# Optimization experiments

Measured on AMD Instinct MI355X. Metric: run time of the kernel, lower is better.

## Reference

```python
import jax, jax.numpy as jnp
import numpy as np

B, N, H, KRATE = 128, 400, 128, 0.2
EPS = 1e-9


def setup_inputs() -> dict:
    key = jax.random.key(0)
    ks = jax.random.split(key, 16)
    # correlation-like input: symmetric, values in (-1,1), unit diagonal
    x = jax.random.normal(ks[0], (B, N, N), dtype=jnp.float32)
    x = jnp.tanh(0.3 * x)
    x = 0.5 * (x + x.transpose(0, 2, 1))
    eye = jnp.eye(N, dtype=jnp.float32)
    x = x * (1.0 - eye) + eye

    def lin(k, fan_in, shape):
        return jax.random.normal(k, shape, dtype=jnp.float32) / np.sqrt(fan_in).astype(np.float32)

    return {
        "x": x,
        "slength": jnp.full((B,), 100, dtype=jnp.int32),
        # AE denoiser (num_of_node=N, hidden=H)
        "enc1_w": lin(ks[1], N, (N, H)), "enc1_b": jnp.zeros((H,), jnp.float32),
        "enc2_w": lin(ks[2], N, (N, H)), "enc2_b": jnp.zeros((H,), jnp.float32),
        "dec2_w": lin(ks[3], H, (H, N)), "dec2_b": jnp.zeros((N,), jnp.float32),
        "dec1_w": lin(ks[4], H, (H, N)), "dec1_b": jnp.zeros((N,), jnp.float32),
        # GCN predictor
        "gcn1_w": lin(ks[5], N, (N, H)), "gcn1_b": jnp.zeros((H,), jnp.float32),
        "gcn2_w": lin(ks[6], H, (H, H)), "gcn2_b": jnp.zeros((H,), jnp.float32),
        # classification head Linear(128 -> 2)
        "fc_w": lin(ks[7], H, (H, 2)), "fc_b": jnp.zeros((2,), jnp.float32),
    }


def reference(x, slength, enc1_w, enc1_b, enc2_w, enc2_b, dec2_w, dec2_b,
              dec1_w, dec1_b, gcn1_w, gcn1_b, gcn2_w, gcn2_b, fc_w, fc_b):
    eye = jnp.eye(N, dtype=x.dtype)

    # fisher transform + normalize by [0,0] entry
    xf = 0.5 * jnp.log((1.0 + x + EPS) / (1.0 - x + EPS))
    xf = xf / xf[:, 0, 0][:, None, None]

    # --- DA / AE denoiser: deltax = AE(xf), symmetrized ---
    out1 = jax.nn.relu(jnp.einsum('bij,jh->bih', xf, enc1_w) + enc1_b).transpose(0, 2, 1)  # [B,H,N]
    out2 = jax.nn.relu(jnp.einsum('bhn,nk->bhk', out1, enc2_w) + enc2_b)                   # [B,H,H]
    out2 = jax.nn.relu(jnp.einsum('bhk,kn->bhn', out2, dec2_w) + dec2_b + out1)            # [B,H,N]
    out2 = out2.transpose(0, 2, 1)                                                         # [B,N,H]
    delta = jnp.einsum('bnh,hm->bnm', out2, dec1_w) + dec1_b                               # [B,N,N]
    delta = 0.5 * (delta + delta.transpose(0, 2, 1))
    x2 = xf + delta * (1.0 - eye)

    # --- predictor on detached x2 ---
    xp = jax.lax.stop_gradient(x2)

    # topk sparsification at rate 0.2 over flattened NxN per sample
    k = int(N * N * KRATE)
    flat = xp.reshape(B, N * N)
    _, idx = jax.lax.top_k(flat, k)
    mask = jnp.zeros((B, N * N), xp.dtype).at[jnp.arange(B)[:, None], idx].set(1.0)
    A = xp * mask.reshape(B, N, N)

    # GCN norm (PyG gcn_norm with add_remaining_self_loops, fill=1)
    diag = jnp.diagonal(A, axis1=1, axis2=2)
    A = A + eye[None] * jnp.where(diag == 0.0, 1.0, 0.0)[:, :, None]
    deg = A.sum(axis=1)                      # scatter of edge weight on col index
    dinv = deg ** -0.5
    dinv = jnp.where(jnp.isinf(dinv), 0.0, dinv)
    An = dinv[:, :, None] * A * dinv[:, None, :]  # An[b,i,j] = dinv[i]*A[i,j]*dinv[j]

    # GCNConv1 -> ReLU -> GCNConv2 (aggregate onto col/target index)
    h = jax.nn.relu(jnp.einsum('bij,bif->bjf', An, xp @ gcn1_w) + gcn1_b)  # [B,N,H]
    h = jnp.einsum('bij,bif->bjf', An, h @ gcn2_w) + gcn2_b                # [B,N,H]

    pooled = h.mean(axis=1)                  # mean over nodes -> [B,H]
    out = jax.nn.relu(pooled) @ fc_w + fc_b  # [B,2]
    return out
```

## Files before the change

kernel.cpp:

```cpp
#include <hip/hip_runtime.h>
#include <hip/hip_bf16.h>
#include <math.h>

#define BATCH 128
#define NNODE 400
#define HID   128
#define NN    (NNODE*NNODE)
#define KSEL  32000
#define EQCAP 1024
#define EPSF  1e-9f
#define TSPLIT 8
#define SEG   (NN / TSPLIT)
#define NT    7
#define KC400 14
#define FRAGS (KC400*4096)
#define PLA   57344

__device__ __forceinline__ unsigned tokey(float f) {
  unsigned u = __float_as_uint(f);
  return (u & 0x80000000u) ? ~u : (u | 0x80000000u);
}

__device__ __forceinline__ short f2bf(float f) {
  unsigned u = __float_as_uint(f);
  u += 0x7fffu + ((u >> 16) & 1u);
  return (short)(u >> 16);
}
__device__ __forceinline__ float bf2f(short s) {
  return __uint_as_float(((unsigned)(unsigned short)s) << 16);
}

__device__ __forceinline__ float xfhw(float xv, float cmul) {
  float la = __builtin_amdgcn_logf(1.0f + xv + EPSF);
  float lb = __builtin_amdgcn_logf(1.0f - xv + EPSF);
  return (la - lb) * cmul;
}

typedef __attribute__((ext_vector_type(8))) short s8v;
typedef __attribute__((ext_vector_type(4))) short s4v;
typedef __attribute__((ext_vector_type(4))) float f4v;

#define BK 16
#define LP 68

template<bool AT, bool BIAS, bool RES, bool RELU, bool TS>
__global__ void __launch_bounds__(256) gemm64(
    const float* __restrict__ A, long sA, int lda,
    const float* __restrict__ B, long sB, int ldb,
    const float* __restrict__ bias,
    const float* __restrict__ Res, long sRes,
    float* __restrict__ C, long sC, int ldc,
    int M, int Nc, int K)
{
  __shared__ float As[BK][LP];
  __shared__ float Bs[BK][LP];
  const int bz = blockIdx.z;
  A += (size_t)bz * sA;
  B += (size_t)bz * sB;
  C += (size_t)bz * sC;
  const float* Rp = RES ? (Res + (size_t)bz * sRes) : nullptr;

  const int n0 = blockIdx.x * 64;
  const int m0 = blockIdx.y * 64;
  const int tid = threadIdx.x;
  const int tx = tid & 15, ty = tid >> 4;
  const bool edgeM = (m0 + 64 > M);
  const bool edgeN = (n0 + 64 > Nc);

  float acc[4][4];
#pragma unroll
  for (int i = 0; i < 4; ++i)
#pragma unroll
    for (int j = 0; j < 4; ++j) acc[i][j] = 0.f;

  for (int k0 = 0; k0 < K; k0 += BK) {
    if (!AT) {
      const int m = tid & 63, g = tid >> 6;
      if (!edgeM) {
        const float4 v = *(const float4*)(A + (size_t)(m0 + m) * lda + k0 + 4 * g);
        As[4 * g + 0][m] = v.x; As[4 * g + 1][m] = v.y;
        As[4 * g + 2][m] = v.z; As[4 * g + 3][m] = v.w;
      } else {
        const int gm = m0 + m;
        const bool ok = gm < M;
#pragma unroll
        for (int j = 0; j < 4; ++j)
          As[4 * g + j][m] = ok ? A[(size_t)gm * lda + k0 + 4 * g + j] : 0.f;
      }
    } else {
      const int k = tid >> 4, mg = tid & 15;
      if (!edgeM) {
        const float4 v = *(const float4*)(A + (size_t)(k0 + k) * lda + m0 + 4 * mg);
        *(float4*)&As[k][4 * mg] = v;
      } else {
#pragma unroll
        for (int j = 0; j < 4; ++j) {
          const int gm = m0 + 4 * mg + j;
          As[k][4 * mg + j] = (gm < M) ? A[(size_t)(k0 + k) * lda + gm] : 0.f;
        }
      }
    }
    {
      const int k = tid >> 4, ng = tid & 15;
      if (!edgeN) {
        const float4 v = *(const float4*)(B + (size_t)(k0 + k) * ldb + n0 + 4 * ng);
        *(float4*)&Bs[k][4 * ng] = v;
      } else {
#pragma unroll
        for (int j = 0; j < 4; ++j) {
          const int gn = n0 + 4 * ng + j;
          Bs[k][4 * ng + j] = (gn < Nc) ? B[(size_t)(k0 + k) * ldb + gn] : 0.f;
        }
      }
    }
    __syncthreads();
#pragma unroll
    for (int kk = 0; kk < BK; ++kk) {
      const float4 a = *(const float4*)&As[kk][ty << 2];
      const float4 b = *(const float4*)&Bs[kk][tx << 2];
      const float av[4] = {a.x, a.y, a.z, a.w};
      const float bv[4] = {b.x, b.y, b.z, b.w};
#pragma unroll
      for (int i = 0; i < 4; ++i)
#pragma unroll
        for (int j = 0; j < 4; ++j) acc[i][j] += av[i] * bv[j];
    }
    __syncthreads();
  }

#pragma unroll
  for (int i = 0; i < 4; ++i) {
    const int m = m0 + (ty << 2) + i;
    if (m >= M) continue;
#pragma unroll
    for (int j = 0; j < 4; ++j) {
      const int n = n0 + (tx << 2) + j;
      if (n >= Nc) continue;
      float v = acc[i][j];
      if (BIAS) v += bias[n];
      const size_t loc = TS ? ((size_t)n * ldc + m) : ((size_t)m * ldc + n);
      if (RES) v += Rp[loc];
      if (RELU) v = fmaxf(v, 0.f);
      C[loc] = v;
    }
  }
}

__global__ void bsplitN(const float* __restrict__ W, int K, int Kpad,
                        int N, int Npad, short* __restrict__ out) {
  int t = blockIdx.x * 256 + threadIdx.x;
  if (t >= Kpad * Npad) return;
  int k = t / Npad, n = t - k * Npad;
  float v = (k < K && n < N) ? W[(size_t)k * N + n] : 0.f;
  short hi = f2bf(v);
  short lo = f2bf(v - bf2f(hi));
  int ntiles = Npad >> 4;
  size_t idx = (((size_t)(k >> 5) * ntiles + (n >> 4)) * 64
                + (((k >> 3) & 3) * 16 + (n & 15))) * 8 + (k & 7);
  size_t PL = (size_t)(Kpad >> 5) * ntiles * 512;
  out[idx] = hi;
  out[PL + idx] = lo;
}

template<bool AT, bool FRAG, bool BIAS, bool RELU, bool SCL, bool TS, bool XF>
__global__ void __launch_bounds__(256) mfgemm(
    const float* __restrict__ A, long sA, int lda,
    const short* __restrict__ Bf, long sB, int kc,
    const float* __restrict__ bias,
    const float* __restrict__ scl,
    float* __restrict__ Cf, long sCf, int ldc,
    short* __restrict__ Cfrag, long sCfrag, int okc,
    const float* __restrict__ denomp, float* __restrict__ xfout,
    int M, int K)
{
  __shared__ float As[64][68];
  const int bz = blockIdx.y;
  A += (size_t)bz * sA;
  Bf += (size_t)bz * sB;
  if (SCL) scl += (size_t)bz * NNODE;
  if (!FRAG) Cf += (size_t)bz * sCf;
  else       Cfrag += (size_t)bz * sCfrag;
  if (XF) xfout += (size_t)bz * sA;
  const float cmul = XF ? (0.34657359027997264f / denomp[bz]) : 0.f;

  const int tid = threadIdx.x;
  const int lane = tid & 63, wave = tid >> 6;
  const int wqm = wave >> 1, wqn = wave & 1;
  const int quad = lane >> 4, l15 = lane & 15;
  const int m0 = blockIdx.x * 64;

  f4v acc[2][4];
#pragma unroll
  for (int i = 0; i < 2; ++i)
#pragma unroll
    for (int j = 0; j < 4; ++j) acc[i][j] = (f4v){0.f, 0.f, 0.f, 0.f};

  const int nstage = (K + 63) >> 6;
  for (int st = 0; st < nstage; ++st) {
    const int k0 = st << 6;
    if (st) __syncthreads();
    if (!AT) {
      const int mrow = tid >> 4;
      const int k4 = (tid & 15) << 2;
#pragma unroll
      for (int u = 0; u < 4; ++u) {
        const int m = mrow + (u << 4);
        const int gm = m0 + m, gk = k0 + k4;
        float4 v = {0.f, 0.f, 0.f, 0.f};
        if (gm < M) {
          if (gk + 4 <= K) {
            float4 xv = *(const float4*)(A + (size_t)gm * lda + gk);
            if (XF) {
              v.x = xfhw(xv.x, cmul);
              v.y = xfhw(xv.y, cmul);
              v.z = xfhw(xv.z, cmul);
              v.w = xfhw(xv.w, cmul);
              *(float4*)(xfout + (size_t)gm * lda + gk) = v;
            } else v = xv;
          } else {
            float* pv = (float*)&v;
#pragma unroll
            for (int j = 0; j < 4; ++j)
              if (gk + j < K) {
                float xv = A[(size_t)gm * lda + gk + j];
                if (XF) {
                  pv[j] = xfhw(xv, cmul);
                  xfout[(size_t)gm * lda + gk + j] = pv[j];
                } else pv[j] = xv;
              }
          }
        }
        *(float4*)&As[m][k4] = v;
      }
    } else {
      const int kk = tid >> 4;
      const int m4 = (tid & 15) << 2;
#pragma unroll
      for (int u = 0; u < 4; ++u) {
        const int gk = k0 + kk + (u << 4);
        float4 v = {0.f, 0.f, 0.f, 0.f};
        if (gk < K) {
          if (m0 + m4 + 4 <= M) v = *(const float4*)(A + (size_t)gk * lda + m0 + m4);
          else {
            float* pv = (float*)&v;
#pragma unroll
            for (int j = 0; j < 4; ++j)
              if (m0 + m4 + j < M) pv[j] = A[(size_t)gk * lda + m0 + m4 + j];
          }
        }
        As[m4 + 0][kk + (u << 4)] = v.x;
        As[m4 + 1][kk + (u << 4)] = v.y;
        As[m4 + 2][kk + (u << 4)] = v.z;
        As[m4 + 3][kk + (u << 4)] = v.w;
      }
    }
    __syncthreads();

#pragma unroll
    for (int c2 = 0; c2 < 2; ++c2) {
      const int c = (st << 1) + c2;
      s8v bhi[4], blo[4];
#pragma unroll
      for (int nt = 0; nt < 4; ++nt) {
        const int ntg = (wqn << 2) + nt;
        const size_t off = (((size_t)c * 8 + ntg) * 64 + lane) * 8;
        bhi[nt] = *(const s8v*)(Bf + off);
        blo[nt] = *(const s8v*)(Bf + (size_t)kc * 4096 + off);
      }
#pragma unroll
      for (int mt = 0; mt < 2; ++mt) {
        const int row = (wqm << 5) + (mt << 4) + l15;
        const int kof = (c2 << 5) + (quad << 3);
        const f4v a0 = *(const f4v*)&As[row][kof];
        const f4v a1 = *(const f4v*)&As[row][kof + 4];
        s8v ah, al;
#pragma unroll
        for (int j = 0; j < 4; ++j) {
          short h0 = f2bf(a0[j]); ah[j] = h0; al[j] = f2bf(a0[j] - bf2f(h0));
          short h1 = f2bf(a1[j]); ah[j + 4] = h1; al[j + 4] = f2bf(a1[j] - bf2f(h1));
        }
#pragma unroll
        for (int nt = 0; nt < 4; ++nt) {
          acc[mt][nt] = __builtin_amdgcn_mfma_f32_16x16x32_bf16(ah, bhi[nt], acc[mt][nt], 0, 0, 0);
          acc[mt][nt] = __builtin_amdgcn_mfma_f32_16x16x32_bf16(ah, blo[nt], acc[mt][nt], 0, 0, 0);
          acc[mt][nt] = __builtin_amdgcn_mfma_f32_16x16x32_bf16(al, bhi[nt], acc[mt][nt], 0, 0, 0);
        }
      }
    }
  }

  if (TS) {
    for (int nh = 0; nh < 2; ++nh) {
      __syncthreads();
      if (wqn == nh) {
#pragma unroll
        for (int mt = 0; mt < 2; ++mt)
#pragma unroll
          for (int nt = 0; nt < 4; ++nt) {
            const int tn = (nt << 4) + l15;
            const int n  = (wqn << 6) + tn;
            const int mc = (wqm << 5) + (mt << 4) + (quad << 2);
            const f4v a = acc[mt][nt];
#pragma unroll
            for (int reg = 0; reg < 4; ++reg) {
              float v = a[reg];
              if (SCL) v *= scl[m0 + mc + reg];
              if (BIAS) v += bias[n];
              if (RELU) v = fmaxf(v, 0.f);
              As[tn][mc + reg] = v;
            }
          }
      }
      __syncthreads();
      const int row = tid >> 2, cq = tid & 3;
#pragma unroll
      for (int u = 0; u < 4; ++u) {
        const int col = (cq + (u << 2)) << 2;
        if (m0 + col + 4 <= M) {
          const float4 v = *(const float4*)&As[row][col];
          *(float4*)(Cf + (size_t)((nh << 6) + row) * ldc + m0 + col) = v;
        }
      }
    }
    return;
  }

#pragma unroll
  for (int mt = 0; mt < 2; ++mt) {
    const int mb = m0 + (wqm << 5) + (mt << 4) + (quad << 2);
#pragma unroll
    for (int nt = 0; nt < 4; ++nt) {
      const int n = (wqn << 6) + (nt << 4) + l15;
      const f4v a = acc[mt][nt];
      if (!FRAG) {
#pragma unroll
        for (int reg = 0; reg < 4; ++reg) {
          const int m = mb + reg;
          if (m < M) {
            float v = a[reg];
            if (SCL) v *= scl[m];
            if (BIAS) v += bias[n];
            if (RELU) v = fmaxf(v, 0.f);
            Cf[(size_t)m * ldc + n] = v;
          }
        }
      } else {
        s4v h4, l4;
#pragma unroll
        for (int reg = 0; reg < 4; ++reg) {
          const int m = mb + reg;
          float v = (m < M) ? (SCL ? a[reg] * scl[m] : a[reg]) : 0.f;
          short hh = f2bf(v);
          h4[reg] = hh; l4[reg] = f2bf(v - bf2f(hh));
        }
        const int chunkT = mb >> 5, quadT = (mb >> 3) & 3, jT0 = mb & 7;
        const size_t off = (((size_t)chunkT * 8 + (wqn << 2) + nt) * 64
                            + quadT * 16 + l15) * 8 + jT0;
        *(s4v*)(Cfrag + off) = h4;
        *(s4v*)(Cfrag + (size_t)okc * 4096 + off) = l4;
      }
    }
  }
}

__global__ void __launch_bounds__(256) g4mf(
    const float* __restrict__ o1,
    const short* __restrict__ wfrag,
    const float* __restrict__ bias,
    float* __restrict__ xf,
    unsigned* __restrict__ ghist)
{
  __shared__ float D2[64][68];
  __shared__ unsigned hist[2304];
  const int b = blockIdx.y;
  int p = blockIdx.x, bi = 0;
  while (p >= NT - bi) { p -= NT - bi; ++bi; }
  const int bj = bi + p;
  const int I0 = bi * 64, J0 = bj * 64;
  const bool diag = (bi == bj);

  o1 += (size_t)b * HID * NNODE;
  xf += (size_t)b * NN;
  unsigned* gh = ghist + b * 256;

  const int tid = threadIdx.x;
  const int lane = tid & 63, wave = tid >> 6;
  const int wq = wave & 1;
  const bool d1 = wave < 2;
  const int Bt = (d1 ? bj : bi) * 4;
  const int quad = lane >> 4, l15 = lane & 15;
  const int M0 = d1 ? I0 : J0;

  for (int i = tid; i < 2304; i += 256) hist[i] = 0u;

  f4v acc[2][4];
#pragma unroll
  for (int i = 0; i < 2; ++i)
#pragma unroll
    for (int j = 0; j < 4; ++j) acc[i][j] = (f4v){0.f, 0.f, 0.f, 0.f};

  const int gm0 = M0 + (wq << 5) + l15;

  for (int c = 0; c < 4; ++c) {
    const int k0 = c << 5;
    s8v bhi[4], blo[4];
#pragma unroll
    for (int nt = 0; nt < 4; ++nt) {
      const int ntg = Bt + nt;
      const size_t off = (((size_t)c * 28 + ntg) * 64 + lane) * 8;
      bhi[nt] = *(const s8v*)(wfrag + off);
      blo[nt] = *(const s8v*)(wfrag + PLA + off);
    }
#pragma unroll
    for (int mt = 0; mt < 2; ++mt) {
      const int gm = gm0 + (mt << 4);
      float av[8];
      if (gm < NNODE) {
        const float* cp = o1 + (size_t)(k0 + (quad << 3)) * NNODE + gm;
#pragma unroll
        for (int j = 0; j < 8; ++j) av[j] = cp[(size_t)j * NNODE];
      } else {
#pragma unroll
        for (int j = 0; j < 8; ++j) av[j] = 0.f;
      }
      s8v ah, al;
#pragma unroll
      for (int j = 0; j < 8; ++j) {
        short h = f2bf(av[j]); ah[j] = h; al[j] = f2bf(av[j] - bf2f(h));
      }
#pragma unroll
      for (int nt = 0; nt < 4; ++nt) {
        acc[mt][nt] = __builtin_amdgcn_mfma_f32_16x16x32_bf16(ah, bhi[nt], acc[mt][nt], 0, 0, 0);
        acc[mt][nt] = __builtin_amdgcn_mfma_f32_16x16x32_bf16(ah, blo[nt], acc[mt][nt], 0, 0, 0);
        acc[mt][nt] = __builtin_amdgcn_mfma_f32_16x16x32_bf16(al, bhi[nt], acc[mt][nt], 0, 0, 0);
      }
    }
  }

  if (!d1) {
#pragma unroll
    for (int mt = 0; mt < 2; ++mt) {
      const int mb = (wq << 5) + (mt << 4) + (quad << 2);
#pragma unroll
      for (int nt = 0; nt < 4; ++nt) {
        const int nn = (nt << 4) + l15;
        const f4v a = acc[mt][nt];
#pragma unroll
        for (int reg = 0; reg < 4; ++reg) D2[mb + reg][nn] = a[reg];
      }
    }
  }
  __syncthreads();

  if (d1) {
    const int rep = tid & 7;
#pragma unroll
    for (int mt = 0; mt < 2; ++mt) {
      const int a0 = (wq << 5) + (mt << 4) + (quad << 2);
#pragma unroll
      for (int nt = 0; nt < 4; ++nt) {
        const int nn = (nt << 4) + l15;
        const int gj = J0 + nn;
        const f4v d1v = acc[mt][nt];
        const f4v d2t = *(const f4v*)&D2[nn][a0];
        f4v vv;
#pragma unroll
        for (int reg = 0; reg < 4; ++reg) {
          const int gi = I0 + a0 + reg;
          float v = 0.f;
          if (gi < NNODE && gj < NNODE) {
            v = xf[(size_t)gi * NNODE + gj];
            if (gi != gj)
              v += 0.5f * (d1v[reg] + d2t[reg] + bias[gj] + bias[gi]);
            atomicAdd(&hist[(tokey(v) >> 24) * 9 + rep], diag ? 1u : 2u);
          }
          vv[reg] = v;
        }
#pragma unroll
        for (int reg = 0; reg < 4; ++reg) {
          const int gi = I0 + a0 + reg;
          if (gi < NNODE && gj < NNODE) xf[(size_t)gi * NNODE + gj] = vv[reg];
        }
        if (!diag && gj < NNODE && (I0 + a0 + 4 <= NNODE)) {
          *(float4*)(xf + (size_t)gj * NNODE + I0 + a0) = *(float4*)&vv;
        }
      }
    }
  }
  __syncthreads();
  if (tid < 256) {
    const int hb = tid * 9;
    const unsigned s = hist[hb + 0] + hist[hb + 1] + hist[hb + 2] + hist[hb + 3]
                     + hist[hb + 4] + hist[hb + 5] + hist[hb + 6] + hist[hb + 7];
    if (s) atomicAdd(&gh[tid], s);
  }
}

__global__ void denom_k(const float* __restrict__ x, float* __restrict__ denom) {
  int b = threadIdx.x;
  if (b < BATCH) {
    float v = x[(size_t)b * NN];
    denom[b] = 0.5f * logf((1.0f + v + EPSF) / (1.0f - v + EPSF));
  }
}

__global__ void tz_init(unsigned* __restrict__ ghist, unsigned* __restrict__ sprefix,
                        int* __restrict__ sk, int* __restrict__ eqcnt,
                        float* __restrict__ deg) {
  int t = blockIdx.x * 256 + threadIdx.x;
  if (t < BATCH * 256) ghist[t] = 0u;
  if (t < BATCH) { sprefix[t] = 0u; sk[t] = KSEL; eqcnt[t] = 0; }
  if (t < BATCH * NNODE) deg[t] = 0.f;
}

template<int PASS>
__global__ void __launch_bounds__(256) thist(const float* __restrict__ x2,
                                             const unsigned* __restrict__ sprefix,
                                             unsigned* __restrict__ ghist) {
  constexpr int shift = 24 - 8 * PASS;
  __shared__ unsigned h[8][256];
  const int b  = blockIdx.y;
  const int sb = blockIdx.x;
  const int tid = threadIdx.x;
  for (int i = tid; i < 8 * 256; i += 256) ((unsigned*)h)[i] = 0u;
  __syncthreads();

  const unsigned prefix = sprefix[b];
  const unsigned pmask  = 0xFFFFFFFFu << (shift + 8);
  const int rep = tid & 7;
  const float4* p4 = (const float4*)(x2 + (size_t)b * NN);
  const int i0 = sb * (SEG / 4), i1 = i0 + (SEG / 4);
  for (int i = i0 + tid; i < i1; i += 256) {
    float4 v = p4[i];
    unsigned k0 = tokey(v.x), k1 = tokey(v.y), k2 = tokey(v.z), k3 = tokey(v.w);
    if ((k0 & pmask) == prefix) atomicAdd(&h[rep][(k0 >> shift) & 255u], 1u);
    if ((k1 & pmask) == prefix) atomicAdd(&h[rep][(k1 >> shift) & 255u], 1u);
    if ((k2 & pmask) == prefix) atomicAdd(&h[rep][(k2 >> shift) & 255u], 1u);
    if ((k3 & pmask) == prefix) atomicAdd(&h[rep][(k3 >> shift) & 255u], 1u);
  }
  __syncthreads();
  if (tid < 256) {
    unsigned s = h[0][tid] + h[1][tid] + h[2][tid] + h[3][tid]
               + h[4][tid] + h[5][tid] + h[6][tid] + h[7][tid];
    if (s) atomicAdd(&ghist[b * 256 + tid], s);
  }
}

template<int PASS>
__global__ void __launch_bounds__(256) tpick(unsigned* __restrict__ ghist,
                                             unsigned* __restrict__ sprefix,
                                             int* __restrict__ sk,
                                             unsigned* __restrict__ tau,
                                             int* __restrict__ rrem) {
  constexpr int shift = 24 - 8 * PASS;
  const int b = blockIdx.x;
  __shared__ unsigned h[256];
  h[threadIdx.x] = ghist[b * 256 + threadIdx.x];
  __syncthreads();
  if (threadIdx.x == 0) {
    int k = sk[b];
    unsigned byte = 0u;
    for (int bin = 255; bin >= 0; --bin) {
      int c = (int)h[bin];
      if (c >= k) { byte = (unsigned)bin; break; }
      k -= c;
    }
    unsigned np = sprefix[b] | (byte << shift);
    sprefix[b] = np; sk[b] = k;
    if (PASS == 3) { tau[b] = np; rrem[b] = k; }
  }
  ghist[b * 256 + threadIdx.x] = 0u;
}

__global__ void __launch_bounds__(256) build_kc(
    const float* __restrict__ x2, const unsigned* __restrict__ tau,
    float* __restrict__ A, float* __restrict__ deg,
    int* __restrict__ eqcnt, int* __restrict__ eqidx) {
  __shared__ float cs[NNODE];
  const int b = blockIdx.y, rg = blockIdx.x;
  const int tid = threadIdx.x;
  for (int i = tid; i < NNODE; i += 256) cs[i] = 0.f;
  __syncthreads();
  const unsigned tk = tau[b];
  const size_t base = (size_t)b * NN + (size_t)rg * 6400;
  for (int u = 0; u < 25; ++u) {
    const int t = u * 256 + tid;
    const float v = x2[base + t];
    const unsigned key = tokey(v);
    const float a = (key > tk) ? v : 0.f;
    A[base + t] = a;
    if (key == tk) {
      int p = atomicAdd(&eqcnt[b], 1);
      if (p < EQCAP) eqidx[b * EQCAP + p] = rg * 6400 + t;
    }
    if (a != 0.f) atomicAdd(&cs[t % NNODE], a);
  }
  __syncthreads();
  for (int j = tid; j < NNODE; j += 256)
    if (cs[j] != 0.f) atomicAdd(&deg[b * NNODE + j], cs[j]);
}

__global__ void eqfix_k(float* __restrict__ A, const float* __restrict__ x2,
                        float* __restrict__ deg,
                        const int* __restrict__ eqcnt, const int* __restrict__ eqidx,
                        const int* __restrict__ rrem) {
  int b = blockIdx.x;
  int cnt = eqcnt[b]; if (cnt > EQCAP) cnt = EQCAP;
  int r = rrem[b];
  for (int t = threadIdx.x; t < cnt; t += 256) {
    int idx = eqidx[b * EQCAP + t];
    int rank = 0;
    for (int u = 0; u < cnt; ++u) rank += (eqidx[b * EQCAP + u] < idx) ? 1 : 0;
    if (rank < r) {
      float v = x2[(size_t)b * NN + idx];
      A[(size_t)b * NN + idx] = v;
      atomicAdd(&deg[b * NNODE + idx % NNODE], v);
    }
  }
}

__global__ void dinv_k(float* __restrict__ A, const float* __restrict__ deg,
                       float* __restrict__ dinv) {
  int t = blockIdx.x * blockDim.x + threadIdx.x;
  if (t >= BATCH * NNODE) return;
  int b = t / NNODE, j = t - b * NNODE;
  float d = deg[t];
  size_t o = (size_t)b * NN + (size_t)j * NNODE + j;
  if (A[o] == 0.f) { A[o] = 1.0f; d += 1.0f; }
  dinv[t] = (d == 0.f) ? 0.f : 1.0f / sqrtf(d);
}

__global__ void head_k(const float* __restrict__ h2, const float* __restrict__ fc_w,
                       const float* __restrict__ fc_b, float* __restrict__ out) {
  int b = blockIdx.x;
  int f = threadIdx.x;
  float s = 0.f;
  const float* p = h2 + (size_t)b * NNODE * HID + f;
  for (int j = 0; j < NNODE; ++j) s += p[(size_t)j * HID];
  float pv = fmaxf(s / (float)NNODE, 0.f);
  __shared__ float r0[128], r1[128];
  r0[f] = pv * fc_w[f * 2 + 0];
  r1[f] = pv * fc_w[f * 2 + 1];
  __syncthreads();
  for (int sft = 64; sft > 0; sft >>= 1) {
    if (f < sft) { r0[f] += r0[f + sft]; r1[f] += r1[f + sft]; }
    __syncthreads();
  }
  if (f == 0) {
    out[b * 2 + 0] = r0[0] + fc_b[0];
    out[b * 2 + 1] = r1[0] + fc_b[1];
  }
}

extern "C" void kernel_launch(void* const* d_in, const int* in_sizes, int n_in,
                              void* d_out, int out_size, void* d_ws, size_t ws_size,
                              hipStream_t stream) {
  const float* x      = (const float*)d_in[0];
  const float* enc1_w = (const float*)d_in[2];
  const float* enc1_b = (const float*)d_in[3];
  const float* enc2_w = (const float*)d_in[4];
  const float* enc2_b = (const float*)d_in[5];
  const float* dec2_w = (const float*)d_in[6];
  const float* dec2_b = (const float*)d_in[7];
  const float* dec1_w = (const float*)d_in[8];
  const float* dec1_b = (const float*)d_in[9];
  const float* gcn1_w = (const float*)d_in[10];
  const float* gcn1_b = (const float*)d_in[11];
  const float* gcn2_w = (const float*)d_in[12];
  const float* gcn2_b = (const float*)d_in[13];
  const float* fc_w   = (const float*)d_in[14];
  const float* fc_b   = (const float*)d_in[15];
  float* out = (float*)d_out;
  (void)in_sizes; (void)n_in; (void)out_size; (void)ws_size;

  float* ws = (float*)d_ws;
  size_t off = 0;
  auto take = [&](size_t n) { float* p = ws + off; off += (n + 63) & ~(size_t)63; return p; };
  float* xf   = take((size_t)BATCH * NN);
  float* dl   = take((size_t)BATCH * NN);
  float* o1   = take((size_t)BATCH * HID * NNODE);
  float* o2   = take((size_t)BATCH * HID * HID);
  float* hbuf = take((size_t)BATCH * NNODE * HID);
  float* denom = take(BATCH);
  float* dinv  = take((size_t)BATCH * NNODE);
  float* deg   = take((size_t)BATCH * NNODE);
  unsigned* tau = (unsigned*)take(BATCH);
  int* rrem  = (int*)take(BATCH);
  int* eqcnt = (int*)take(BATCH);
  int* eqidx = (int*)take((size_t)BATCH * EQCAP);
  unsigned* ghist   = (unsigned*)take((size_t)BATCH * 256);
  unsigned* sprefix = (unsigned*)take(BATCH);
  int*      sk      = (int*)take(BATCH);
  short* w1frag = (short*)take((size_t)FRAGS + 64);
  short* w2frag = (short*)take((size_t)4 * 4096 + 64);
  short* e1frag = (short*)take((size_t)FRAGS + 64);
  short* e2frag = (short*)take((size_t)FRAGS + 64);
  short* dfrag  = (short*)take((size_t)PLA + 64);
  short* xwfrag = (short*)o1;
  const long sXW = 2L * FRAGS;

  tz_init<<<200, 256, 0, stream>>>(ghist, sprefix, sk, eqcnt, deg);
  denom_k<<<1, BATCH, 0, stream>>>(x, denom);
  bsplitN<<<224, 256, 0, stream>>>(gcn1_w, NNODE, 448, HID, 128, w1frag);
  bsplitN<<<64,  256, 0, stream>>>(gcn2_w, HID, 128, HID, 128, w2frag);
  bsplitN<<<224, 256, 0, stream>>>(enc1_w, NNODE, 448, HID, 128, e1frag);
  bsplitN<<<224, 256, 0, stream>>>(enc2_w, NNODE, 448, HID, 128, e2frag);
  bsplitN<<<224, 256, 0, stream>>>(dec1_w, HID, 128, NNODE, 448, dfrag);

  mfgemm<false, false, true, true, false, true, true><<<dim3(7, BATCH), 256, 0, stream>>>(
      x, NN, NNODE, e1frag, 0, KC400, enc1_b, nullptr,
      o1, (long)HID * NNODE, NNODE, nullptr, 0, 0, denom, xf, NNODE, NNODE);
  mfgemm<false, false, true, true, false, false, false><<<dim3(2, BATCH), 256, 0, stream>>>(
      o1, (long)HID * NNODE, NNODE, e2frag, 0, KC400, enc2_b, nullptr,
      o2, (long)HID * HID, HID, nullptr, 0, 0, nullptr, nullptr, HID, NNODE);
  gemm64<false, true, true, true, false><<<dim3(7, 2, BATCH), 256, 0, stream>>>(
      o2, (long)HID * HID, HID, dec2_w, 0, NNODE, dec2_b,
      o1, (long)HID * NNODE, o1, (long)HID * NNODE, NNODE, HID, NNODE, HID);

  g4mf<<<dim3(NT * (NT + 1) / 2, BATCH), 256, 0, stream>>>(o1, dfrag, dec1_b, xf, ghist);

  tpick<0><<<BATCH, 256, 0, stream>>>(ghist, sprefix, sk, tau, rrem);
  thist<1><<<dim3(TSPLIT, BATCH), 256, 0, stream>>>(xf, sprefix, ghist);
  tpick<1><<<BATCH, 256, 0, stream>>>(ghist, sprefix, sk, tau, rrem);
  thist<2><<<dim3(TSPLIT, BATCH), 256, 0, stream>>>(xf, sprefix, ghist);
  tpick<2><<<BATCH, 256, 0, stream>>>(ghist, sprefix, sk, tau, rrem);
  thist<3><<<dim3(TSPLIT, BATCH), 256, 0, stream>>>(xf, sprefix, ghist);
  tpick<3><<<BATCH, 256, 0, stream>>>(ghist, sprefix, sk, tau, rrem);

  build_kc<<<dim3(25, BATCH), 256, 0, stream>>>(xf, tau, dl, deg, eqcnt, eqidx);
  eqfix_k<<<BATCH, 256, 0, stream>>>(dl, xf, deg, eqcnt, eqidx, rrem);
  dinv_k<<<(BATCH * NNODE + 255) / 256, 256, 0, stream>>>(dl, deg, dinv);

  mfgemm<false, true, false, false, true, false, false><<<dim3(7, BATCH), 256, 0, stream>>>(
      xf, NN, NNODE, w1frag, 0, KC400, nullptr, dinv,
      nullptr, 0, 128, xwfrag, sXW, KC400, nullptr, nullptr, NNODE, NNODE);
  mfgemm<true, false, true, true, true, false, false><<<dim3(7, BATCH), 256, 0, stream>>>(
      dl, NN, NNODE, xwfrag, sXW, KC400, gcn1_b, dinv,
      hbuf, (long)NNODE * HID, HID, nullptr, 0, 0, nullptr, nullptr, NNODE, NNODE);
  mfgemm<false, true, false, false, true, false, false><<<dim3(7, BATCH), 256, 0, stream>>>(
      hbuf, (long)NNODE * HID, HID, w2frag, 0, 4, nullptr, dinv,
      nullptr, 0, 128, xwfrag, sXW, KC400, nullptr, nullptr, NNODE, HID);
  mfgemm<true, false, true, false, true, false, false><<<dim3(7, BATCH), 256, 0, stream>>>(
      dl, NN, NNODE, xwfrag, sXW, KC400, gcn2_b, dinv,
      hbuf, (long)NNODE * HID, HID, nullptr, 0, 0, nullptr, nullptr, NNODE, NNODE);

  head_k<<<BATCH, HID, 0, stream>>>(hbuf, fc_w, fc_b, out);
}
```

Baseline: 665.8 us.

## Switch top-k radix select to 12/12/8-bit passes and fuse small setup kernels

The radix threshold search now uses 4096-bin histograms for the first two digits (12 bits each) and 256 bins for the last byte. This cuts the passes over the 160k-element matrix from three to two, and the number of tpick launches from four to three. Initialization, denominator, the five weight-split kernels, and eqfix/dinv are each merged into single launches to reduce launch overhead. In exchange, ghist grows 16x and must be zeroed and scanned, and the first-pass shared histogram in g4mf loses its 8-way replication, which risks more atomic contention.

After: 653.3 us. No clear change (-1.9%).

```diff
diff --git a/kernel.cpp b/kernel.cpp
--- a/kernel.cpp
+++ b/kernel.cpp
@@ -146,8 +146,21 @@
   }
 }
 
-__global__ void bsplitN(const float* __restrict__ W, int K, int Kpad,
-                        int N, int Npad, short* __restrict__ out) {
+__global__ void bsplit5(
+    const float* __restrict__ gcn1_w, const float* __restrict__ gcn2_w,
+    const float* __restrict__ enc1_w, const float* __restrict__ enc2_w,
+    const float* __restrict__ dec1_w,
+    short* __restrict__ w1frag, short* __restrict__ w2frag,
+    short* __restrict__ e1frag, short* __restrict__ e2frag,
+    short* __restrict__ dfrag) {
+  const float* W; short* out; int K, Kpad, N, Npad;
+  switch (blockIdx.y) {
+    case 0: W = gcn1_w; out = w1frag; K = NNODE; Kpad = 448; N = HID;   Npad = 128; break;
+    case 1: W = gcn2_w; out = w2frag; K = HID;   Kpad = 128; N = HID;   Npad = 128; break;
+    case 2: W = enc1_w; out = e1frag; K = NNODE; Kpad = 448; N = HID;   Npad = 128; break;
+    case 3: W = enc2_w; out = e2frag; K = NNODE; Kpad = 448; N = HID;   Npad = 128; break;
+    default: W = dec1_w; out = dfrag; K = HID;   Kpad = 128; N = NNODE; Npad = 448; break;
+  }
   int t = blockIdx.x * 256 + threadIdx.x;
   if (t >= Kpad * Npad) return;
   int k = t / Npad, n = t - k * Npad;
@@ -371,7 +384,7 @@
     unsigned* __restrict__ ghist)
 {
   __shared__ float D2[64][68];
-  __shared__ unsigned hist[2304];
+  __shared__ unsigned hist[4096];
   const int b = blockIdx.y;
   int p = blockIdx.x, bi = 0;
   while (p >= NT - bi) { p -= NT - bi; ++bi; }
@@ -381,7 +394,7 @@
 
   o1 += (size_t)b * HID * NNODE;
   xf += (size_t)b * NN;
-  unsigned* gh = ghist + b * 256;
+  unsigned* gh = ghist + (size_t)b * 4096;
 
   const int tid = threadIdx.x;
   const int lane = tid & 63, wave = tid >> 6;
@@ -391,7 +404,7 @@
   const int quad = lane >> 4, l15 = lane & 15;
   const int M0 = d1 ? I0 : J0;
 
-  for (int i = tid; i < 2304; i += 256) hist[i] = 0u;
+  for (int i = tid; i < 4096; i += 256) hist[i] = 0u;
 
   f4v acc[2][4];
 #pragma unroll
@@ -453,7 +466,6 @@
   __syncthreads();
 
   if (d1) {
-    const int rep = tid & 7;
 #pragma unroll
     for (int mt = 0; mt < 2; ++mt) {
       const int a0 = (wq << 5) + (mt << 4) + (quad << 2);
@@ -472,7 +484,7 @@
             v = xf[(size_t)gi * NNODE + gj];
             if (gi != gj)
               v += 0.5f * (d1v[reg] + d2t[reg] + bias[gj] + bias[gi]);
-            atomicAdd(&hist[(tokey(v) >> 24) * 9 + rep], diag ? 1u : 2u);
+            atomicAdd(&hist[tokey(v) >> 20], diag ? 1u : 2u);
           }
           vv[reg] = v;
         }
@@ -488,36 +500,57 @@
     }
   }
   __syncthreads();
-  if (tid < 256) {
-    const int hb = tid * 9;
-    const unsigned s = hist[hb + 0] + hist[hb + 1] + hist[hb + 2] + hist[hb + 3]
-                     + hist[hb + 4] + hist[hb + 5] + hist[hb + 6] + hist[hb + 7];
-    if (s) atomicAdd(&gh[tid], s);
-  }
-}
-
-__global__ void denom_k(const float* __restrict__ x, float* __restrict__ denom) {
-  int b = threadIdx.x;
-  if (b < BATCH) {
-    float v = x[(size_t)b * NN];
-    denom[b] = 0.5f * logf((1.0f + v + EPSF) / (1.0f - v + EPSF));
-  }
-}
-
-__global__ void tz_init(unsigned* __restrict__ ghist, unsigned* __restrict__ sprefix,
-                        int* __restrict__ sk, int* __restrict__ eqcnt,
-                        float* __restrict__ deg) {
+  for (int i = tid; i < 4096; i += 256) {
+    const unsigned s = hist[i];
+    if (s) atomicAdd(&gh[i], s);
+  }
+}
+
+__global__ void tzd(const float* __restrict__ x, unsigned* __restrict__ ghist,
+                    unsigned* __restrict__ sprefix, int* __restrict__ sk,
+                    int* __restrict__ eqcnt, float* __restrict__ deg,
+                    float* __restrict__ denom) {
   int t = blockIdx.x * 256 + threadIdx.x;
-  if (t < BATCH * 256) ghist[t] = 0u;
-  if (t < BATCH) { sprefix[t] = 0u; sk[t] = KSEL; eqcnt[t] = 0; }
+  if (t < BATCH * 4096) ghist[t] = 0u;
+  if (t < BATCH) {
+    sprefix[t] = 0u; sk[t] = KSEL; eqcnt[t] = 0;
+    float v = x[(size_t)t * NN];
+    denom[t] = 0.5f * logf((1.0f + v + EPSF) / (1.0f - v + EPSF));
+  }
   if (t < BATCH * NNODE) deg[t] = 0.f;
 }
 
-template<int PASS>
-__global__ void __launch_bounds__(256) thist(const float* __restrict__ x2,
-                                             const unsigned* __restrict__ sprefix,
-                                             unsigned* __restrict__ ghist) {
-  constexpr int shift = 24 - 8 * PASS;
+__global__ void __launch_bounds__(256) thistA(const float* __restrict__ x2,
+                                              const unsigned* __restrict__ sprefix,
+                                              unsigned* __restrict__ ghist) {
+  __shared__ unsigned h[4096];
+  const int b  = blockIdx.y;
+  const int sb = blockIdx.x;
+  const int tid = threadIdx.x;
+  for (int i = tid; i < 4096; i += 256) h[i] = 0u;
+  __syncthreads();
+
+  const unsigned prefix = sprefix[b];
+  const float4* p4 = (const float4*)(x2 + (size_t)b * NN);
+  const int i0 = sb * (SEG / 4), i1 = i0 + (SEG / 4);
+  for (int i = i0 + tid; i < i1; i += 256) {
+    float4 v = p4[i];
+    unsigned k0 = tokey(v.x), k1 = tokey(v.y), k2 = tokey(v.z), k3 = tokey(v.w);
+    if ((k0 & 0xFFF00000u) == prefix) atomicAdd(&h[(k0 >> 8) & 4095u], 1u);
+    if ((k1 & 0xFFF00000u) == prefix) atomicAdd(&h[(k1 >> 8) & 4095u], 1u);
+    if ((k2 & 0xFFF00000u) == prefix) atomicAdd(&h[(k2 >> 8) & 4095u], 1u);
+    if ((k3 & 0xFFF00000u) == prefix) atomicAdd(&h[(k3 >> 8) & 4095u], 1u);
+  }
+  __syncthreads();
+  for (int i = tid; i < 4096; i += 256) {
+    unsigned s = h[i];
+    if (s) atomicAdd(&ghist[(size_t)b * 4096 + i], s);
+  }
+}
+
+__global__ void __launch_bounds__(256) thistB(const float* __restrict__ x2,
+                                              const unsigned* __restrict__ sprefix,
+                                              unsigned* __restrict__ ghist) {
   __shared__ unsigned h[8][256];
   const int b  = blockIdx.y;
   const int sb = blockIdx.x;
@@ -526,36 +559,72 @@
   __syncthreads();
 
   const unsigned prefix = sprefix[b];
-  const unsigned pmask  = 0xFFFFFFFFu << (shift + 8);
   const int rep = tid & 7;
   const float4* p4 = (const float4*)(x2 + (size_t)b * NN);
   const int i0 = sb * (SEG / 4), i1 = i0 + (SEG / 4);
   for (int i = i0 + tid; i < i1; i += 256) {
     float4 v = p4[i];
     unsigned k0 = tokey(v.x), k1 = tokey(v.y), k2 = tokey(v.z), k3 = tokey(v.w);
-    if ((k0 & pmask) == prefix) atomicAdd(&h[rep][(k0 >> shift) & 255u], 1u);
-    if ((k1 & pmask) == prefix) atomicAdd(&h[rep][(k1 >> shift) & 255u], 1u);
-    if ((k2 & pmask) == prefix) atomicAdd(&h[rep][(k2 >> shift) & 255u], 1u);
-    if ((k3 & pmask) == prefix) atomicAdd(&h[rep][(k3 >> shift) & 255u], 1u);
+    if ((k0 & 0xFFFFFF00u) == prefix) atomicAdd(&h[rep][k0 & 255u], 1u);
+    if ((k1 & 0xFFFFFF00u) == prefix) atomicAdd(&h[rep][k1 & 255u], 1u);
+    if ((k2 & 0xFFFFFF00u) == prefix) atomicAdd(&h[rep][k2 & 255u], 1u);
+    if ((k3 & 0xFFFFFF00u) == prefix) atomicAdd(&h[rep][k3 & 255u], 1u);
   }
   __syncthreads();
   if (tid < 256) {
     unsigned s = h[0][tid] + h[1][tid] + h[2][tid] + h[3][tid]
                + h[4][tid] + h[5][tid] + h[6][tid] + h[7][tid];
-    if (s) atomicAdd(&ghist[b * 256 + tid], s);
-  }
-}
-
-template<int PASS>
-__global__ void __launch_bounds__(256) tpick(unsigned* __restrict__ ghist,
-                                             unsigned* __restrict__ sprefix,
-                                             int* __restrict__ sk,
-                                             unsigned* __restrict__ tau,
-                                             int* __restrict__ rrem) {
-  constexpr int shift = 24 - 8 * PASS;
+    if (s) atomicAdd(&ghist[(size_t)b * 4096 + tid], s);
+  }
+}
+
+template<int SH>
+__global__ void __launch_bounds__(256) tpick12(unsigned* __restrict__ ghist,
+                                               unsigned* __restrict__ sprefix,
+                                               int* __restrict__ sk) {
+  const int b = blockIdx.x;
+  __shared__ unsigned h[4096];
+  __shared__ unsigned csum[256];
+  unsigned* gh = ghist + (size_t)b * 4096;
+  unsigned local = 0;
+#pragma unroll
+  for (int u = 0; u < 16; ++u) {
+    unsigned v = gh[threadIdx.x * 16 + u];
+    h[threadIdx.x * 16 + u] = v;
+    local += v;
+  }
+  csum[threadIdx.x] = local;
+  __syncthreads();
+  if (threadIdx.x == 0) {
+    int k = sk[b];
+    int bin = 0;
+    for (int ch = 255; ch >= 0; --ch) {
+      int S = (int)csum[ch];
+      if (S >= k) {
+        for (int bb = ch * 16 + 15; bb >= ch * 16; --bb) {
+          int c = (int)h[bb];
+          if (c >= k) { bin = bb; break; }
+          k -= c;
+        }
+        break;
+      }
+      k -= S;
+    }
+    sprefix[b] = sprefix[b] | ((unsigned)bin << SH);
+    sk[b] = k;
+  }
+#pragma unroll
+  for (int u = 0; u < 16; ++u) gh[threadIdx.x * 16 + u] = 0u;
+}
+
+__global__ void __launch_bounds__(256) tpick8f(const unsigned* __restrict__ ghist,
+                                               const unsigned* __restrict__ sprefix,
+                                               const int* __restrict__ sk,
+                                               unsigned* __restrict__ tau,
+                                               int* __restrict__ rrem) {
   const int b = blockIdx.x;
   __shared__ unsigned h[256];
-  h[threadIdx.x] = ghist[b * 256 + threadIdx.x];
+  h[threadIdx.x] = ghist[(size_t)b * 4096 + threadIdx.x];
   __syncthreads();
   if (threadIdx.x == 0) {
     int k = sk[b];
@@ -565,11 +634,9 @@
       if (c >= k) { byte = (unsigned)bin; break; }
       k -= c;
     }
-    unsigned np = sprefix[b] | (byte << shift);
-    sprefix[b] = np; sk[b] = k;
-    if (PASS == 3) { tau[b] = np; rrem[b] = k; }
-  }
-  ghist[b * 256 + threadIdx.x] = 0u;
+    tau[b] = sprefix[b] | byte;
+    rrem[b] = k;
+  }
 }
 
 __global__ void __launch_bounds__(256) build_kc(
@@ -600,13 +667,14 @@
     if (cs[j] != 0.f) atomicAdd(&deg[b * NNODE + j], cs[j]);
 }
 
-__global__ void eqfix_k(float* __restrict__ A, const float* __restrict__ x2,
-                        float* __restrict__ deg,
-                        const int* __restrict__ eqcnt, const int* __restrict__ eqidx,
-                        const int* __restrict__ rrem) {
-  int b = blockIdx.x;
+__global__ void __launch_bounds__(256) eqdinv(
+    float* __restrict__ A, const float* __restrict__ x2,
+    float* __restrict__ deg, float* __restrict__ dinv,
+    const int* __restrict__ eqcnt, const int* __restrict__ eqidx,
+    const int* __restrict__ rrem) {
+  const int b = blockIdx.x;
   int cnt = eqcnt[b]; if (cnt > EQCAP) cnt = EQCAP;
-  int r = rrem[b];
+  const int r = rrem[b];
   for (int t = threadIdx.x; t < cnt; t += 256) {
     int idx = eqidx[b * EQCAP + t];
     int rank = 0;
@@ -617,17 +685,13 @@
       atomicAdd(&deg[b * NNODE + idx % NNODE], v);
     }
   }
-}
-
-__global__ void dinv_k(float* __restrict__ A, const float* __restrict__ deg,
-                       float* __restrict__ dinv) {
-  int t = blockIdx.x * blockDim.x + threadIdx.x;
-  if (t >= BATCH * NNODE) return;
-  int b = t / NNODE, j = t - b * NNODE;
-  float d = deg[t];
-  size_t o = (size_t)b * NN + (size_t)j * NNODE + j;
-  if (A[o] == 0.f) { A[o] = 1.0f; d += 1.0f; }
-  dinv[t] = (d == 0.f) ? 0.f : 1.0f / sqrtf(d);
+  __syncthreads();
+  for (int j = threadIdx.x; j < NNODE; j += 256) {
+    float d = deg[b * NNODE + j];
+    size_t o = (size_t)b * NN + (size_t)j * NNODE + j;
+    if (A[o] == 0.f) { A[o] = 1.0f; d += 1.0f; }
+    dinv[b * NNODE + j] = (d == 0.f) ? 0.f : 1.0f / sqrtf(d);
+  }
 }
 
 __global__ void head_k(const float* __restrict__ h2, const float* __restrict__ fc_w,
@@ -688,7 +752,7 @@
   int* rrem  = (int*)take(BATCH);
   int* eqcnt = (int*)take(BATCH);
   int* eqidx = (int*)take((size_t)BATCH * EQCAP);
-  unsigned* ghist   = (unsigned*)take((size_t)BATCH * 256);
+  unsigned* ghist   = (unsigned*)take((size_t)BATCH * 4096);
   unsigned* sprefix = (unsigned*)take(BATCH);
   int*      sk      = (int*)take(BATCH);
   short* w1frag = (short*)take((size_t)FRAGS + 64);
@@ -699,13 +763,9 @@
   short* xwfrag = (short*)o1;
   const long sXW = 2L * FRAGS;
 
-  tz_init<<<200, 256, 0, stream>>>(ghist, sprefix, sk, eqcnt, deg);
-  denom_k<<<1, BATCH, 0, stream>>>(x, denom);
-  bsplitN<<<224, 256, 0, stream>>>(gcn1_w, NNODE, 448, HID, 128, w1frag);
-  bsplitN<<<64,  256, 0, stream>>>(gcn2_w, HID, 128, HID, 128, w2frag);
-  bsplitN<<<224, 256, 0, stream>>>(enc1_w, NNODE, 448, HID, 128, e1frag);
-  bsplitN<<<224, 256, 0, stream>>>(enc2_w, NNODE, 448, HID, 128, e2frag);
-  bsplitN<<<224, 256, 0, stream>>>(dec1_w, HID, 128, NNODE, 448, dfrag);
+  tzd<<<2048, 256, 0, stream>>>(x, ghist, sprefix, sk, eqcnt, deg, denom);
+  bsplit5<<<dim3(224, 5), 256, 0, stream>>>(gcn1_w, gcn2_w, enc1_w, enc2_w, dec1_w,
+                                            w1frag, w2frag, e1frag, e2frag, dfrag);
 
   mfgemm<false, false, true, true, false, true, true><<<dim3(7, BATCH), 256, 0, stream>>>(
       x, NN, NNODE, e1frag, 0, KC400, enc1_b, nullptr,
@@ -719,17 +779,14 @@
 
   g4mf<<<dim3(NT * (NT + 1) / 2, BATCH), 256, 0, stream>>>(o1, dfrag, dec1_b, xf, ghist);
 
-  tpick<0><<<BATCH, 256, 0, stream>>>(ghist, sprefix, sk, tau, rrem);
-  thist<1><<<dim3(TSPLIT, BATCH), 256, 0, stream>>>(xf, sprefix, ghist);
-  tpick<1><<<BATCH, 256, 0, stream>>>(ghist, sprefix, sk, tau, rrem);
-  thist<2><<<dim3(TSPLIT, BATCH), 256, 0, stream>>>(xf, sprefix, ghist);
-  tpick<2><<<BATCH, 256, 0, stream>>>(ghist, sprefix, sk, tau, rrem);
-  thist<3><<<dim3(TSPLIT, BATCH), 256, 0, stream>>>(xf, sprefix, ghist);
-  tpick<3><<<BATCH, 256, 0, stream>>>(ghist, sprefix, sk, tau, rrem);
+  tpick12<20><<<BATCH, 256, 0, stream>>>(ghist, sprefix, sk);
+  thistA<<<dim3(TSPLIT, BATCH), 256, 0, stream>>>(xf, sprefix, ghist);
+  tpick12<8><<<BATCH, 256, 0, stream>>>(ghist, sprefix, sk);
+  thistB<<<dim3(TSPLIT, BATCH), 256, 0, stream>>>(xf, sprefix, ghist);
+  tpick8f<<<BATCH, 256, 0, stream>>>(ghist, sprefix, sk, tau, rrem);
 
   build_kc<<<dim3(25, BATCH), 256, 0, stream>>>(xf, tau, dl, deg, eqcnt, eqidx);
-  eqfix_k<<<BATCH, 256, 0, stream>>>(dl, xf, deg, eqcnt, eqidx, rrem);
-  dinv_k<<<(BATCH * NNODE + 255) / 256, 256, 0, stream>>>(dl, deg, dinv);
+  eqdinv<<<BATCH, 256, 0, stream>>>(dl, xf, deg, dinv, eqcnt, eqidx, rrem);
 
   mfgemm<false, true, false, false, true, false, false><<<dim3(7, BATCH), 256, 0, stream>>>(
       xf, NN, NNODE, w1frag, 0, KC400, nullptr, dinv,
```
